# Optimization experiments

Hardware: AMD Instinct MI355X
Metric: run time of the kernel (lower is better)

The kernel has to match this reference:

```python
import jax, jax.numpy as jnp
import numpy as np

B, RES, C = 32, 56, 128
HEADS, WS, NW = 4, 7, 8
HD = C // HEADS            # 32
NQ = NW * NW               # 64 windows
WA = WS * WS               # 49 tokens per window
TOPK = 64


def _topk_closest(q_win, k_win, topk):
    qh, qw = q_win; kh, kw = k_win
    ch_q = np.arange(qh); cw_q = np.arange(qw)
    if qh != kh:
        f = kh // qh
        ch_q = ch_q * f + f // 2
        cw_q = cw_q * f + f // 2
    cq = np.stack(np.meshgrid(ch_q, cw_q, indexing='ij'))              # (2,qh,qw)
    ck = np.stack(np.meshgrid(np.arange(kh), np.arange(kw), indexing='ij'))
    fq = cq.reshape(2, -1); fk = ck.reshape(2, -1)
    rel = fq[:, :, None] - fk[:, None, :]                               # (2,nQ,nK)
    dist = np.sqrt(rel[0].astype(np.float32) ** 2 + rel[1].astype(np.float32) ** 2)
    topk = min(topk, dist.shape[1])
    idx = np.argsort(dist, axis=1, kind='stable')[:, :topk]             # (nQ,topk)
    coord = np.take_along_axis(rel, np.broadcast_to(idx[None], (2,) + idx.shape), axis=2)
    return idx.astype(np.int32), coord.transpose(1, 2, 0).astype(np.float32)


def _buffers():
    # window-relative coords, same as register_buffer('window_coords')
    ch = np.arange(WS) - WS // 2
    wc = np.stack(np.meshgrid(ch, ch, indexing='ij'), axis=-1).reshape(-1, 2).astype(np.float32)  # (49,2)
    # level 0: fine grid (RES x RES); level 1: window grid (NW x NW)
    idx0, c0 = _topk_closest((NW, NW), (RES, RES), TOPK)
    idx1, c1 = _topk_closest((NW, NW), (NW, NW), TOPK)
    c1 = c1 * WS  # k > 0 coords scaled by window size
    coords0 = c0[:, None, :, :] + wc[None, :, None, :]   # (NQ,49,TOPK,2)
    coords1 = c1[:, None, :, :] + wc[None, :, None, :]
    return idx0, idx1, coords0, coords1


def setup_inputs() -> dict:
    key = jax.random.key(0)
    ks = jax.random.split(key, 16)
    idx0, idx1, coords0, coords1 = _buffers()
    s = 0.02
    return {
        'x0': jax.random.normal(ks[0], (B, RES, RES, C), jnp.float32),
        'x1': jax.random.normal(ks[1], (B, NQ, C), jnp.float32),
        'qkv_w': jax.random.normal(ks[2], (3 * C, C), jnp.float32) * s,
        'qkv_b': jnp.zeros((3 * C,), jnp.float32),
        'proj_w': jax.random.normal(ks[3], (C, C), jnp.float32) * s,
        'proj_b': jnp.zeros((C,), jnp.float32),
        'rpb0_w1': jax.random.normal(ks[4], (HD, 2), jnp.float32) * s,
        'rpb0_b1': jnp.zeros((HD,), jnp.float32),
        'rpb0_w2': jax.random.normal(ks[5], (HEADS, HD), jnp.float32) * s,
        'rpb0_b2': jnp.zeros((HEADS,), jnp.float32),
        'rpb1_w1': jax.random.normal(ks[6], (HD, 2), jnp.float32) * s,
        'rpb1_b1': jnp.zeros((HD,), jnp.float32),
        'rpb1_w2': jax.random.normal(ks[7], (HEADS, HD), jnp.float32) * s,
        'rpb1_b2': jnp.zeros((HEADS,), jnp.float32),
        'coords0': jnp.asarray(coords0),
        'coords1': jnp.asarray(coords1),
        'idx0': jnp.asarray(idx0),
        'idx1': jnp.asarray(idx1),
    }


def _rpb_mlp(coords, w1, b1, w2, b2):
    # (NQ,49,T,2) -> (NQ,49,T,heads)
    return jax.nn.relu(coords @ w1.T + b1) @ w2.T + b2


def _gather_kv(kv, idx_flat):
    # kv: (B,L,heads,hd); gathered -> (B,NQ,heads,TOPK,hd)
    g = kv[:, idx_flat]
    return g.reshape(kv.shape[0], NQ, TOPK, HEADS, HD).transpose(0, 1, 3, 2, 4)


def reference(x0, x1, qkv_w, qkv_b, proj_w, proj_b,
              rpb0_w1, rpb0_b1, rpb0_w2, rpb0_b2,
              rpb1_w1, rpb1_b1, rpb1_w2, rpb1_b2,
              coords0, coords1, idx0, idx1):
    b = x0.shape[0]
    scale = HD ** -0.5
    qkv = x0 @ qkv_w.T + qkv_b                       # (B,RES,RES,3C)
    q, k, v = jnp.split(qkv, 3, axis=-1)
    # window-partition q: (B,RES,RES,C) -> (B,NQ,heads,49,hd)
    qw = q.reshape(b, NW, WS, NW, WS, C).transpose(0, 1, 3, 2, 4, 5)
    qw = qw.reshape(b, NQ, WA, HEADS, HD).transpose(0, 1, 3, 2, 4)
    # level 0 KV from fine grid
    k0 = k.reshape(b, RES * RES, HEADS, HD)
    v0 = v.reshape(b, RES * RES, HEADS, HD)
    i0 = idx0.reshape(-1)
    k0s, v0s = _gather_kv(k0, i0), _gather_kv(v0, i0)
    # level 1 KV from pooled tokens (same qkv projection)
    qkv1 = (x1 @ qkv_w.T + qkv_b).reshape(b, NQ, 3, HEADS, HD)
    i1 = idx1.reshape(-1)
    k1s, v1s = _gather_kv(qkv1[:, :, 1], i1), _gather_kv(qkv1[:, :, 2], i1)
    k_all = jnp.concatenate([k0s, k1s], axis=3)      # (B,NQ,heads,2T,hd)
    v_all = jnp.concatenate([v0s, v1s], axis=3)
    attn = jnp.einsum('bqhnd,bqhmd->bqhnm', qw * scale, k_all)  # (B,NQ,heads,49,2T)
    rpb0 = _rpb_mlp(coords0, rpb0_w1, rpb0_b1, rpb0_w2, rpb0_b2)
    rpb1 = _rpb_mlp(coords1, rpb1_w1, rpb1_b1, rpb1_w2, rpb1_b2)
    rpb = jnp.concatenate([rpb0, rpb1], axis=2).transpose(0, 3, 1, 2)  # (NQ,heads,49,2T)
    attn = jax.nn.softmax(attn + rpb[None], axis=-1)
    out = jnp.einsum('bqhnm,bqhmd->bqhnd', attn, v_all)
    out = out.transpose(0, 1, 3, 2, 4).reshape(b * NQ, WA, C)
    return out @ proj_w.T + proj_b
```

## Files before the change

kernel.cpp:

```cpp
#include <hip/hip_runtime.h>
#include <hip/hip_bf16.h>


typedef __bf16 bf16_t;
typedef __bf16 bf16x8 __attribute__((ext_vector_type(8)));
typedef float f32x4 __attribute__((ext_vector_type(4)));

static __device__ __forceinline__ f32x4 mfma_bf16(bf16x8 a, bf16x8 b, f32x4 c) {
  return __builtin_amdgcn_mfma_f32_16x16x32_bf16(a, b, c, 0, 0, 0);
}

static __device__ __forceinline__ bf16x8 cvt8(const float* __restrict__ p) {
  float4 a = *(const float4*)p;
  float4 b = *(const float4*)(p + 4);
  bf16x8 r;
  r[0] = (bf16_t)a.x; r[1] = (bf16_t)a.y; r[2] = (bf16_t)a.z; r[3] = (bf16_t)a.w;
  r[4] = (bf16_t)b.x; r[5] = (bf16_t)b.y; r[6] = (bf16_t)b.z; r[7] = (bf16_t)b.w;
  return r;
}

#define NB 32
#define RES 56
#define CH 128
#define NW 8
#define NQ 64
#define WA 49
#define X0_ROWS (NB * RES * RES)
#define SCALE 0.17677669529663687f
#define SQRT32 5.656854249492381f

__global__ __launch_bounds__(256) void k_qkv(
    const float* __restrict__ x0, const float* __restrict__ x1,
    const float* __restrict__ w, const float* __restrict__ bias,
    bf16_t* __restrict__ qout,
    bf16_t* __restrict__ k0, bf16_t* __restrict__ v0,
    bf16_t* __restrict__ k1, bf16_t* __restrict__ v1) {
  __shared__ __align__(16) bf16_t Asm[64][136];
  __shared__ __align__(16) bf16_t Bsm[128][136];
  const int rb = blockIdx.x;
  const int tid = threadIdx.x;
  const size_t row0 = (size_t)rb * 64;
  const bool is_x0 = (rb < 1568);
  const int b_ = rb / 49;
  const int pix0 = (rb - b_ * 49) * 64;
  const int i1base = (rb - 1568) * 64;

  const float* src = is_x0 ? (x0 + row0 * CH)
                           : (x1 + (row0 - X0_ROWS) * CH);
#pragma unroll
  for (int i = 0; i < 4; ++i) {
    int uid = tid + 256 * i;
    int r = uid >> 4, cs = uid & 15;
    *(bf16x8*)&Asm[r][cs * 8] = cvt8(src + (size_t)r * CH + cs * 8);
  }

  const int wid = tid >> 6, l = tid & 63;
  const int lr = l & 15, lkg = l >> 4, lk = lkg * 8;

  for (int cb = 0; cb < 3; ++cb) {
    const float* wsrc = w + (size_t)cb * 128 * CH;
#pragma unroll
    for (int i = 0; i < 8; ++i) {
      int uid = tid + 256 * i;
      int r = uid >> 4, cs = uid & 15;
      *(bf16x8*)&Bsm[r][cs * 8] = cvt8(wsrc + (size_t)r * CH + cs * 8);
    }
    __syncthreads();

    f32x4 zero = {0.f, 0.f, 0.f, 0.f};
    f32x4 acc[8];
#pragma unroll
    for (int nt = 0; nt < 8; ++nt) acc[nt] = zero;
#pragma unroll
    for (int ks = 0; ks < 4; ++ks) {
      bf16x8 a = *(const bf16x8*)&Asm[wid * 16 + lr][ks * 32 + lk];
#pragma unroll
      for (int nt = 0; nt < 8; ++nt) {
        bf16x8 b = *(const bf16x8*)&Bsm[nt * 16 + lr][ks * 32 + lk];
        acc[nt] = mfma_bf16(a, b, acc[nt]);
      }
    }
    float bias_v[8];
#pragma unroll
    for (int nt = 0; nt < 8; ++nt) bias_v[nt] = bias[cb * 128 + nt * 16 + lr];

#pragma unroll
    for (int r4 = 0; r4 < 4; ++r4) {
      int local = wid * 16 + lkg * 4 + r4;
      if (is_x0) {
        int pix = pix0 + local;
        int rr = pix / 56, cc = pix - rr * 56;
        if (cb == 0) {
          int wn = b_ * 64 + (rr / 7) * 8 + cc / 7;
          int nidx = (rr % 7) * 7 + (cc % 7);
          bf16_t* dst = qout + (size_t)wn * 12544 + nidx * 128;
#pragma unroll
          for (int nt = 0; nt < 8; ++nt)
            dst[nt * 16 + lr] = (bf16_t)(acc[nt][r4] + bias_v[nt]);
        } else {
          bf16_t* dst = (cb == 1 ? k0 : v0) +
                        ((size_t)b_ * 3136 + pix) * CH;
#pragma unroll
          for (int nt = 0; nt < 8; ++nt)
            dst[nt * 16 + lr] = (bf16_t)(acc[nt][r4] + bias_v[nt]);
        }
      } else if (cb != 0) {
        bf16_t* dst = (cb == 1 ? k1 : v1) + (size_t)(i1base + local) * CH;
#pragma unroll
        for (int nt = 0; nt < 8; ++nt)
          dst[nt * 16 + lr] = (bf16_t)(acc[nt][r4] + bias_v[nt]);
      }
    }
    __syncthreads();
  }
}

__global__ __launch_bounds__(256) void k_rpb(
    const float* __restrict__ c0, const float* __restrict__ c1,
    const float* __restrict__ w10, const float* __restrict__ b10,
    const float* __restrict__ w20, const float* __restrict__ b20,
    const float* __restrict__ w11, const float* __restrict__ b11,
    const float* __restrict__ w21, const float* __restrict__ b21,
    float* __restrict__ rpb) {
  __shared__ float w1s[2][32][2], b1s[2][32], w2s[2][4][32], b2s[2][4];
  const int tid = threadIdx.x;
  if (tid < 64) {
    int s = tid >> 5, j = tid & 31;
    const float* w1p = s ? w11 : w10;
    const float* b1p = s ? b11 : b10;
    w1s[s][j][0] = w1p[j * 2];
    w1s[s][j][1] = w1p[j * 2 + 1];
    b1s[s][j] = b1p[j];
  }
  {
    int s = tid >> 7, rem = tid & 127, h = rem >> 5, j = rem & 31;
    w2s[s][h][j] = s ? w21[h * 32 + j] : w20[h * 32 + j];
  }
  if (tid < 8) {
    int s = tid >> 2, h = tid & 3;
    b2s[s][h] = s ? b21[h] : b20[h];
  }
  __syncthreads();

  int L = blockIdx.x * 256 + tid;
  int m = L & 127;
  int n = (L >> 7) % WA;
  int qi = L / (128 * WA);
  int s = m >> 6, mi = m & 63;
  const float* cp = (s ? c1 : c0) + (((size_t)qi * WA + n) * 64 + mi) * 2;
  float cx = cp[0], cy = cp[1];
  float a0 = 0.f, a1 = 0.f, a2 = 0.f, a3 = 0.f;
#pragma unroll
  for (int j = 0; j < 32; ++j) {
    float h = fmaxf(w1s[s][j][0] * cx + w1s[s][j][1] * cy + b1s[s][j], 0.f);
    a0 += w2s[s][0][j] * h;
    a1 += w2s[s][1][j] * h;
    a2 += w2s[s][2][j] * h;
    a3 += w2s[s][3][j] * h;
  }
  size_t base = ((size_t)qi * 4 * WA + n) * 128 + m;
  rpb[base] = (a0 + b2s[s][0]) * SQRT32;
  rpb[base + (size_t)WA * 128] = (a1 + b2s[s][1]) * SQRT32;
  rpb[base + (size_t)2 * WA * 128] = (a2 + b2s[s][2]) * SQRT32;
  rpb[base + (size_t)3 * WA * 128] = (a3 + b2s[s][3]) * SQRT32;
}

__global__ __launch_bounds__(256) void k_attn(
    const bf16_t* qin,
    const bf16_t* __restrict__ k0, const bf16_t* __restrict__ v0,
    const bf16_t* __restrict__ k1, const bf16_t* __restrict__ v1,
    const int* __restrict__ idx0, const int* __restrict__ idx1,
    const float* __restrict__ rpb,
    float* attn_out) {
  __shared__ __align__(16) bf16_t Kt[128][72];
  __shared__ __align__(16) bf16_t Vt[64][136];
  __shared__ __align__(16) bf16_t Sm[64][136];

  const int bid = blockIdx.x;
  const int hp = bid & 1;
  const int qi = (bid >> 1) & 63;
  const int b = bid >> 7;
  const int tid = threadIdx.x;
  const int wn = b * 64 + qi;

#pragma unroll
  for (int i = 0; i < 4; ++i) {
    int uid = tid + 256 * i;
    int key = uid & 127, seg = uid >> 7;
    size_t srcrow;
    const bf16_t *kbase, *vbase;
    if (key < 64) {
      srcrow = (size_t)b * 3136 + idx0[qi * 64 + key];
      kbase = k0; vbase = v0;
    } else {
      srcrow = (size_t)b * 64 + idx1[qi * 64 + key - 64];
      kbase = k1; vbase = v1;
    }
    size_t off = srcrow * CH + hp * 64 + seg * 8;
    *(uint4*)&Kt[key][seg * 8] = *(const uint4*)(kbase + off);
    union { uint4 u; bf16_t h[8]; } cv;
    cv.u = *(const uint4*)(vbase + off);
#pragma unroll
    for (int e = 0; e < 8; ++e) Vt[seg * 8 + e][key] = cv.h[e];
  }

  const int wid = tid >> 6, l = tid & 63;
  const int lr = l & 15, lkg = l >> 4, lk = lkg * 8;
  int qr = wid * 16 + lr;
  if (qr > WA - 1) qr = WA - 1;

  const bf16_t* qb = qin + (size_t)wn * 12544;
  bf16x8 qf[2];
  qf[0] = *(const bf16x8*)&qb[qr * 128 + hp * 64 + lk];
  qf[1] = *(const bf16x8*)&qb[qr * 128 + hp * 64 + 32 + lk];
  __syncthreads();

  const int myrow = wid * 16 + lkg * 4;
  float* obase = attn_out + (size_t)wn * 6272;

#pragma unroll
  for (int lh = 0; lh < 2; ++lh) {
    const int hh = hp * 2 + lh;
    const float* rp = rpb + ((size_t)(qi * 4 + hh) * WA) * 128;
    f32x4 acc[8];
#pragma unroll
    for (int nt = 0; nt < 8; ++nt) {
#pragma unroll
      for (int r4 = 0; r4 < 4; ++r4)
        acc[nt][r4] = rp[(myrow + r4) * 128 + nt * 16 + lr];
    }
#pragma unroll
    for (int nt = 0; nt < 8; ++nt) {
      bf16x8 bfr = *(const bf16x8*)&Kt[nt * 16 + lr][lh * 32 + lk];
      acc[nt] = mfma_bf16(qf[lh], bfr, acc[nt]);
    }
    float mx[4] = {-1e30f, -1e30f, -1e30f, -1e30f};
#pragma unroll
    for (int nt = 0; nt < 8; ++nt)
#pragma unroll
      for (int r4 = 0; r4 < 4; ++r4) mx[r4] = fmaxf(mx[r4], acc[nt][r4]);
#pragma unroll
    for (int m = 1; m < 16; m <<= 1)
#pragma unroll
      for (int r4 = 0; r4 < 4; ++r4)
        mx[r4] = fmaxf(mx[r4], __shfl_xor(mx[r4], m));
    float sum[4] = {0.f, 0.f, 0.f, 0.f};
#pragma unroll
    for (int nt = 0; nt < 8; ++nt)
#pragma unroll
      for (int r4 = 0; r4 < 4; ++r4) {
        float p = __expf(SCALE * (acc[nt][r4] - mx[r4]));
        acc[nt][r4] = p;
        sum[r4] += p;
      }
#pragma unroll
    for (int m = 1; m < 16; m <<= 1)
#pragma unroll
      for (int r4 = 0; r4 < 4; ++r4) sum[r4] += __shfl_xor(sum[r4], m);
#pragma unroll
    for (int nt = 0; nt < 8; ++nt)
#pragma unroll
      for (int r4 = 0; r4 < 4; ++r4)
        Sm[myrow + r4][nt * 16 + lr] = (bf16_t)acc[nt][r4];
    f32x4 zero = {0.f, 0.f, 0.f, 0.f};
    f32x4 oacc[2];
    oacc[0] = zero; oacc[1] = zero;
#pragma unroll
    for (int ks = 0; ks < 4; ++ks) {
      bf16x8 pa = *(const bf16x8*)&Sm[wid * 16 + lr][ks * 32 + lk];
#pragma unroll
      for (int nt2 = 0; nt2 < 2; ++nt2) {
        bf16x8 vb = *(const bf16x8*)&Vt[lh * 32 + nt2 * 16 + lr][ks * 32 + lk];
        oacc[nt2] = mfma_bf16(pa, vb, oacc[nt2]);
      }
    }
#pragma unroll
    for (int nt2 = 0; nt2 < 2; ++nt2)
#pragma unroll
      for (int r4 = 0; r4 < 4; ++r4) {
        int rown = myrow + r4;
        if (rown < WA)
          obase[rown * 128 + hh * 32 + nt2 * 16 + lr] = oacc[nt2][r4] / sum[r4];
      }
  }
}

__global__ __launch_bounds__(256) void k_proj(
    const float* attn,
    const float* __restrict__ pw, const float* __restrict__ pb,
    float* out) {
  __shared__ __align__(16) bf16_t Asm[64][136];
  __shared__ __align__(16) bf16_t Bsm[128][136];
  const int rb = blockIdx.x;
  const int tid = threadIdx.x;
  const size_t row0 = (size_t)rb * 64;
#pragma unroll
  for (int i = 0; i < 4; ++i) {
    int uid = tid + 256 * i;
    int r = uid >> 4, cs = uid & 15;
    *(bf16x8*)&Asm[r][cs * 8] = cvt8(attn + (row0 + r) * CH + cs * 8);
  }
#pragma unroll
  for (int i = 0; i < 8; ++i) {
    int uid = tid + 256 * i;
    int r = uid >> 4, cs = uid & 15;
    *(bf16x8*)&Bsm[r][cs * 8] = cvt8(pw + (size_t)r * CH + cs * 8);
  }
  __syncthreads();

  const int wid = tid >> 6, l = tid & 63;
  const int lr = l & 15, lkg = l >> 4, lk = lkg * 8;
  f32x4 zero = {0.f, 0.f, 0.f, 0.f};
  f32x4 acc[8];
#pragma unroll
  for (int nt = 0; nt < 8; ++nt) acc[nt] = zero;
#pragma unroll
  for (int ks = 0; ks < 4; ++ks) {
    bf16x8 a = *(const bf16x8*)&Asm[wid * 16 + lr][ks * 32 + lk];
#pragma unroll
    for (int nt = 0; nt < 8; ++nt) {
      bf16x8 b = *(const bf16x8*)&Bsm[nt * 16 + lr][ks * 32 + lk];
      acc[nt] = mfma_bf16(a, b, acc[nt]);
    }
  }
#pragma unroll
  for (int nt = 0; nt < 8; ++nt) {
    int n = nt * 16 + lr;
    float bs = pb[n];
#pragma unroll
    for (int r4 = 0; r4 < 4; ++r4) {
      size_t g = row0 + (size_t)(wid * 16 + lkg * 4 + r4);
      out[g * CH + n] = acc[nt][r4] + bs;
    }
  }
}

extern "C" void kernel_launch(void* const* d_in, const int* in_sizes, int n_in,
                              void* d_out, int out_size, void* d_ws, size_t ws_size,
                              hipStream_t stream) {
  const float* x0 = (const float*)d_in[0];
  const float* x1 = (const float*)d_in[1];
  const float* qkv_w = (const float*)d_in[2];
  const float* qkv_b = (const float*)d_in[3];
  const float* proj_w = (const float*)d_in[4];
  const float* proj_b = (const float*)d_in[5];
  const float* rpb0_w1 = (const float*)d_in[6];
  const float* rpb0_b1 = (const float*)d_in[7];
  const float* rpb0_w2 = (const float*)d_in[8];
  const float* rpb0_b2 = (const float*)d_in[9];
  const float* rpb1_w1 = (const float*)d_in[10];
  const float* rpb1_b1 = (const float*)d_in[11];
  const float* rpb1_w2 = (const float*)d_in[12];
  const float* rpb1_b2 = (const float*)d_in[13];
  const float* coords0 = (const float*)d_in[14];
  const float* coords1 = (const float*)d_in[15];
  const int* idx0 = (const int*)d_in[16];
  const int* idx1 = (const int*)d_in[17];

  char* ws = (char*)d_ws;
  bf16_t* k0 = (bf16_t*)(ws + 0);
  bf16_t* v0 = (bf16_t*)(ws + 25690112);
  bf16_t* k1 = (bf16_t*)(ws + 51380224);
  bf16_t* v1 = (bf16_t*)(ws + 51904512);
  float* rpb = (float*)(ws + 52428800);

  k_qkv<<<1600, 256, 0, stream>>>(x0, x1, qkv_w, qkv_b,
                                  (bf16_t*)d_out, k0, v0, k1, v1);
  k_rpb<<<1568, 256, 0, stream>>>(coords0, coords1, rpb0_w1, rpb0_b1, rpb0_w2,
                                  rpb0_b2, rpb1_w1, rpb1_b1, rpb1_w2, rpb1_b2,
                                  rpb);
  k_attn<<<4096, 256, 0, stream>>>((const bf16_t*)d_out, k0, v0, k1, v1,
                                   idx0, idx1, rpb, (float*)d_out);
  k_proj<<<1568, 256, 0, stream>>>((const float*)d_out, proj_w, proj_b,
                                   (float*)d_out);
}
```

Baseline: 228.3 us.

## Fuse output projection into attention and pre-convert weights and RPB to bf16

Adds a prep kernel that converts the qkv and proj weights to bf16 once per call. The rpb table is now stored in bf16, pre-swizzled into the MFMA accumulator layout so it loads as vectors. The qkv GEMM keeps A fragments in registers and stages each output tile through LDS for coalesced 16-byte stores. The attention kernel now handles all four heads of a window per block and applies the output projection in-kernel, which removes the fp32 intermediate round trip and the separate proj launch. The trade-offs are fewer attention blocks (half as many), more LDS per block, and bf16 rounding of the rpb and the attention output before projection.

```diff
diff --git a/kernel.cpp b/kernel.cpp
--- a/kernel.cpp
+++ b/kernel.cpp
@@ -4,6 +4,7 @@
 
 typedef __bf16 bf16_t;
 typedef __bf16 bf16x8 __attribute__((ext_vector_type(8)));
+typedef __bf16 bf16x4 __attribute__((ext_vector_type(4)));
 typedef float f32x4 __attribute__((ext_vector_type(4)));
 
 static __device__ __forceinline__ f32x4 mfma_bf16(bf16x8 a, bf16x8 b, f32x4 c) {
@@ -22,16 +23,76 @@
 #define NB 32
 #define RES 56
 #define CH 128
-#define NW 8
 #define NQ 64
 #define WA 49
 #define X0_ROWS (NB * RES * RES)
 #define SCALE 0.17677669529663687f
 #define SQRT32 5.656854249492381f
 
+__global__ __launch_bounds__(256) void k_prep(
+    const float* __restrict__ qkv_w, const float* __restrict__ proj_w,
+    bf16_t* __restrict__ wq, bf16_t* __restrict__ pwb) {
+  int i = blockIdx.x * 256 + threadIdx.x;
+  if (i < 49152) wq[i] = (bf16_t)qkv_w[i];
+  else if (i - 49152 < 16384) pwb[i - 49152] = (bf16_t)proj_w[i - 49152];
+}
+
+__global__ __launch_bounds__(256) void k_rpb(
+    const float* __restrict__ c0, const float* __restrict__ c1,
+    const float* __restrict__ w10, const float* __restrict__ b10,
+    const float* __restrict__ w20, const float* __restrict__ b20,
+    const float* __restrict__ w11, const float* __restrict__ b11,
+    const float* __restrict__ w21, const float* __restrict__ b21,
+    bf16_t* __restrict__ rpb2) {
+  __shared__ float w1s[2][32][2], b1s[2][32], w2s[2][4][32], b2s[2][4];
+  const int tid = threadIdx.x;
+  if (tid < 64) {
+    int s = tid >> 5, j = tid & 31;
+    const float* w1p = s ? w11 : w10;
+    const float* b1p = s ? b11 : b10;
+    w1s[s][j][0] = w1p[j * 2];
+    w1s[s][j][1] = w1p[j * 2 + 1];
+    b1s[s][j] = b1p[j];
+  }
+  {
+    int s = tid >> 7, rem = tid & 127, h = rem >> 5, j = rem & 31;
+    w2s[s][h][j] = s ? w21[h * 32 + j] : w20[h * 32 + j];
+  }
+  if (tid < 8) {
+    int s = tid >> 2, h = tid & 3;
+    b2s[s][h] = s ? b21[h] : b20[h];
+  }
+  __syncthreads();
+
+  int L = blockIdx.x * 256 + tid;
+  int m = L & 127;
+  int n = (L >> 7) % WA;
+  int qi = L / (128 * WA);
+  int s = m >> 6, mi = m & 63;
+  const float* cp = (s ? c1 : c0) + (((size_t)qi * WA + n) * 64 + mi) * 2;
+  float cx = cp[0], cy = cp[1];
+  float a0 = 0.f, a1 = 0.f, a2 = 0.f, a3 = 0.f;
+#pragma unroll
+  for (int j = 0; j < 32; ++j) {
+    float h = fmaxf(w1s[s][j][0] * cx + w1s[s][j][1] * cy + b1s[s][j], 0.f);
+    a0 += w2s[s][0][j] * h;
+    a1 += w2s[s][1][j] * h;
+    a2 += w2s[s][2][j] * h;
+    a3 += w2s[s][3][j] * h;
+  }
+  int nt = m >> 4, lr = m & 15;
+  int wid2 = n >> 4, lkg2 = (n >> 2) & 3, r4 = n & 3;
+  int t2 = wid2 * 64 + lkg2 * 16 + lr;
+  size_t base2 = (((size_t)(qi * 4) * 8 + nt) * 256 + t2) * 4 + r4;
+  rpb2[base2]         = (bf16_t)((a0 + b2s[s][0]) * SQRT32);
+  rpb2[base2 + 8192]  = (bf16_t)((a1 + b2s[s][1]) * SQRT32);
+  rpb2[base2 + 16384] = (bf16_t)((a2 + b2s[s][2]) * SQRT32);
+  rpb2[base2 + 24576] = (bf16_t)((a3 + b2s[s][3]) * SQRT32);
+}
+
 __global__ __launch_bounds__(256) void k_qkv(
     const float* __restrict__ x0, const float* __restrict__ x1,
-    const float* __restrict__ w, const float* __restrict__ bias,
+    const bf16_t* __restrict__ wq, const float* __restrict__ bias,
     bf16_t* __restrict__ qout,
     bf16_t* __restrict__ k0, bf16_t* __restrict__ v0,
     bf16_t* __restrict__ k1, bf16_t* __restrict__ v1) {
@@ -53,116 +114,80 @@
     int r = uid >> 4, cs = uid & 15;
     *(bf16x8*)&Asm[r][cs * 8] = cvt8(src + (size_t)r * CH + cs * 8);
   }
+#pragma unroll
+  for (int i = 0; i < 8; ++i) {
+    int uid = tid + 256 * i;
+    int r = uid >> 4, cs = uid & 15;
+    *(uint4*)&Bsm[r][cs * 8] = *(const uint4*)(wq + (size_t)r * CH + cs * 8);
+  }
+  __syncthreads();
 
   const int wid = tid >> 6, l = tid & 63;
   const int lr = l & 15, lkg = l >> 4, lk = lkg * 8;
+  const int myrow = wid * 16 + lkg * 4;
+
+  bf16x8 af[4];
+#pragma unroll
+  for (int ks = 0; ks < 4; ++ks)
+    af[ks] = *(const bf16x8*)&Asm[wid * 16 + lr][ks * 32 + lk];
 
   for (int cb = 0; cb < 3; ++cb) {
-    const float* wsrc = w + (size_t)cb * 128 * CH;
-#pragma unroll
-    for (int i = 0; i < 8; ++i) {
-      int uid = tid + 256 * i;
-      int r = uid >> 4, cs = uid & 15;
-      *(bf16x8*)&Bsm[r][cs * 8] = cvt8(wsrc + (size_t)r * CH + cs * 8);
-    }
-    __syncthreads();
-
     f32x4 zero = {0.f, 0.f, 0.f, 0.f};
     f32x4 acc[8];
 #pragma unroll
     for (int nt = 0; nt < 8; ++nt) acc[nt] = zero;
 #pragma unroll
-    for (int ks = 0; ks < 4; ++ks) {
-      bf16x8 a = *(const bf16x8*)&Asm[wid * 16 + lr][ks * 32 + lk];
+    for (int ks = 0; ks < 4; ++ks)
 #pragma unroll
       for (int nt = 0; nt < 8; ++nt) {
         bf16x8 b = *(const bf16x8*)&Bsm[nt * 16 + lr][ks * 32 + lk];
-        acc[nt] = mfma_bf16(a, b, acc[nt]);
-      }
-    }
-    float bias_v[8];
-#pragma unroll
-    for (int nt = 0; nt < 8; ++nt) bias_v[nt] = bias[cb * 128 + nt * 16 + lr];
-
-#pragma unroll
-    for (int r4 = 0; r4 < 4; ++r4) {
-      int local = wid * 16 + lkg * 4 + r4;
-      if (is_x0) {
-        int pix = pix0 + local;
-        int rr = pix / 56, cc = pix - rr * 56;
-        if (cb == 0) {
+        acc[nt] = mfma_bf16(af[ks], b, acc[nt]);
+      }
+    __syncthreads();
+
+    const bool emit = is_x0 || cb != 0;
+    if (emit) {
+#pragma unroll
+      for (int nt = 0; nt < 8; ++nt) {
+        float bs = bias[cb * 128 + nt * 16 + lr];
+#pragma unroll
+        for (int r4 = 0; r4 < 4; ++r4)
+          Asm[myrow + r4][nt * 16 + lr] = (bf16_t)(acc[nt][r4] + bs);
+      }
+    }
+    __syncthreads();
+
+    if (cb < 2) {
+#pragma unroll
+      for (int i = 0; i < 8; ++i) {
+        int uid = tid + 256 * i;
+        int r = uid >> 4, cs = uid & 15;
+        *(uint4*)&Bsm[r][cs * 8] =
+            *(const uint4*)(wq + (size_t)(cb + 1) * 16384 + r * CH + cs * 8);
+      }
+    }
+    if (emit) {
+#pragma unroll
+      for (int i = 0; i < 4; ++i) {
+        int uid = tid + 256 * i;
+        int r = uid >> 4, cs = uid & 15;
+        bf16_t* dptr;
+        if (!is_x0) {
+          dptr = (cb == 1 ? k1 : v1) + (size_t)(i1base + r) * CH;
+        } else if (cb == 0) {
+          int pix = pix0 + r;
+          int rr = pix / 56, cc = pix - rr * 56;
           int wn = b_ * 64 + (rr / 7) * 8 + cc / 7;
-          int nidx = (rr % 7) * 7 + (cc % 7);
-          bf16_t* dst = qout + (size_t)wn * 12544 + nidx * 128;
-#pragma unroll
-          for (int nt = 0; nt < 8; ++nt)
-            dst[nt * 16 + lr] = (bf16_t)(acc[nt][r4] + bias_v[nt]);
+          int nid = (rr % 7) * 7 + (cc % 7);
+          dptr = qout + (size_t)wn * 12544 + nid * 128;
         } else {
-          bf16_t* dst = (cb == 1 ? k0 : v0) +
-                        ((size_t)b_ * 3136 + pix) * CH;
-#pragma unroll
-          for (int nt = 0; nt < 8; ++nt)
-            dst[nt * 16 + lr] = (bf16_t)(acc[nt][r4] + bias_v[nt]);
+          dptr = (cb == 1 ? k0 : v0) + (row0 + r) * CH;
         }
-      } else if (cb != 0) {
-        bf16_t* dst = (cb == 1 ? k1 : v1) + (size_t)(i1base + local) * CH;
-#pragma unroll
-        for (int nt = 0; nt < 8; ++nt)
-          dst[nt * 16 + lr] = (bf16_t)(acc[nt][r4] + bias_v[nt]);
-      }
-    }
-    __syncthreads();
-  }
-}
-
-__global__ __launch_bounds__(256) void k_rpb(
-    const float* __restrict__ c0, const float* __restrict__ c1,
-    const float* __restrict__ w10, const float* __restrict__ b10,
-    const float* __restrict__ w20, const float* __restrict__ b20,
-    const float* __restrict__ w11, const float* __restrict__ b11,
-    const float* __restrict__ w21, const float* __restrict__ b21,
-    float* __restrict__ rpb) {
-  __shared__ float w1s[2][32][2], b1s[2][32], w2s[2][4][32], b2s[2][4];
-  const int tid = threadIdx.x;
-  if (tid < 64) {
-    int s = tid >> 5, j = tid & 31;
-    const float* w1p = s ? w11 : w10;
-    const float* b1p = s ? b11 : b10;
-    w1s[s][j][0] = w1p[j * 2];
-    w1s[s][j][1] = w1p[j * 2 + 1];
-    b1s[s][j] = b1p[j];
-  }
-  {
-    int s = tid >> 7, rem = tid & 127, h = rem >> 5, j = rem & 31;
-    w2s[s][h][j] = s ? w21[h * 32 + j] : w20[h * 32 + j];
-  }
-  if (tid < 8) {
-    int s = tid >> 2, h = tid & 3;
-    b2s[s][h] = s ? b21[h] : b20[h];
-  }
-  __syncthreads();
-
-  int L = blockIdx.x * 256 + tid;
-  int m = L & 127;
-  int n = (L >> 7) % WA;
-  int qi = L / (128 * WA);
-  int s = m >> 6, mi = m & 63;
-  const float* cp = (s ? c1 : c0) + (((size_t)qi * WA + n) * 64 + mi) * 2;
-  float cx = cp[0], cy = cp[1];
-  float a0 = 0.f, a1 = 0.f, a2 = 0.f, a3 = 0.f;
-#pragma unroll
-  for (int j = 0; j < 32; ++j) {
-    float h = fmaxf(w1s[s][j][0] * cx + w1s[s][j][1] * cy + b1s[s][j], 0.f);
-    a0 += w2s[s][0][j] * h;
-    a1 += w2s[s][1][j] * h;
-    a2 += w2s[s][2][j] * h;
-    a3 += w2s[s][3][j] * h;
-  }
-  size_t base = ((size_t)qi * 4 * WA + n) * 128 + m;
-  rpb[base] = (a0 + b2s[s][0]) * SQRT32;
-  rpb[base + (size_t)WA * 128] = (a1 + b2s[s][1]) * SQRT32;
-  rpb[base + (size_t)2 * WA * 128] = (a2 + b2s[s][2]) * SQRT32;
-  rpb[base + (size_t)3 * WA * 128] = (a3 + b2s[s][3]) * SQRT32;
+        *(uint4*)(dptr + cs * 8) = *(const uint4*)&Asm[r][cs * 8];
+      }
+    }
+    __syncthreads();
+  }
 }
 
 __global__ __launch_bounds__(256) void k_attn(
@@ -170,167 +195,162 @@
     const bf16_t* __restrict__ k0, const bf16_t* __restrict__ v0,
     const bf16_t* __restrict__ k1, const bf16_t* __restrict__ v1,
     const int* __restrict__ idx0, const int* __restrict__ idx1,
-    const float* __restrict__ rpb,
+    const bf16_t* __restrict__ rpb2, const bf16_t* __restrict__ pw,
+    const float* __restrict__ pb,
     float* attn_out) {
-  __shared__ __align__(16) bf16_t Kt[128][72];
-  __shared__ __align__(16) bf16_t Vt[64][136];
-  __shared__ __align__(16) bf16_t Sm[64][136];
+  __shared__ __align__(16) char smem[53248];
+  bf16_t* Kt = (bf16_t*)smem;
+  bf16_t* Vt = (bf16_t*)(smem + 18432);
+  bf16_t* Sm = (bf16_t*)(smem + 35840);
+  bf16_t* Om = (bf16_t*)smem;
+  bf16_t* Pw = (bf16_t*)(smem + 18432);
 
   const int bid = blockIdx.x;
-  const int hp = bid & 1;
-  const int qi = (bid >> 1) & 63;
-  const int b = bid >> 7;
+  const int qi = bid & 63;
+  const int b = bid >> 6;
   const int tid = threadIdx.x;
-  const int wn = b * 64 + qi;
-
-#pragma unroll
-  for (int i = 0; i < 4; ++i) {
-    int uid = tid + 256 * i;
-    int key = uid & 127, seg = uid >> 7;
-    size_t srcrow;
-    const bf16_t *kbase, *vbase;
-    if (key < 64) {
-      srcrow = (size_t)b * 3136 + idx0[qi * 64 + key];
-      kbase = k0; vbase = v0;
-    } else {
-      srcrow = (size_t)b * 64 + idx1[qi * 64 + key - 64];
-      kbase = k1; vbase = v1;
-    }
-    size_t off = srcrow * CH + hp * 64 + seg * 8;
-    *(uint4*)&Kt[key][seg * 8] = *(const uint4*)(kbase + off);
-    union { uint4 u; bf16_t h[8]; } cv;
-    cv.u = *(const uint4*)(vbase + off);
-#pragma unroll
-    for (int e = 0; e < 8; ++e) Vt[seg * 8 + e][key] = cv.h[e];
-  }
+  const int wn = bid;
 
   const int wid = tid >> 6, l = tid & 63;
   const int lr = l & 15, lkg = l >> 4, lk = lkg * 8;
+  const int myrow = wid * 16 + lkg * 4;
   int qr = wid * 16 + lr;
   if (qr > WA - 1) qr = WA - 1;
-
   const bf16_t* qb = qin + (size_t)wn * 12544;
-  bf16x8 qf[2];
-  qf[0] = *(const bf16x8*)&qb[qr * 128 + hp * 64 + lk];
-  qf[1] = *(const bf16x8*)&qb[qr * 128 + hp * 64 + 32 + lk];
-  __syncthreads();
-
-  const int myrow = wid * 16 + lkg * 4;
-  float* obase = attn_out + (size_t)wn * 6272;
-
-#pragma unroll
-  for (int lh = 0; lh < 2; ++lh) {
-    const int hh = hp * 2 + lh;
-    const float* rp = rpb + ((size_t)(qi * 4 + hh) * WA) * 128;
-    f32x4 acc[8];
-#pragma unroll
-    for (int nt = 0; nt < 8; ++nt) {
+
+  f32x4 oreg[4][2];
+  float rsum[4][4];
+
+  for (int p = 0; p < 2; ++p) {
+#pragma unroll
+    for (int i = 0; i < 4; ++i) {
+      int uid = tid + 256 * i;
+      int key = uid & 127, seg = uid >> 7;
+      size_t srcrow;
+      const bf16_t *kbase, *vbase;
+      if (key < 64) {
+        srcrow = (size_t)b * 3136 + idx0[qi * 64 + key];
+        kbase = k0; vbase = v0;
+      } else {
+        srcrow = (size_t)b * 64 + idx1[qi * 64 + key - 64];
+        kbase = k1; vbase = v1;
+      }
+      size_t off = srcrow * CH + p * 64 + seg * 8;
+      *(uint4*)&Kt[key * 72 + seg * 8] = *(const uint4*)(kbase + off);
+      union { uint4 u; bf16_t h[8]; } cv;
+      cv.u = *(const uint4*)(vbase + off);
+#pragma unroll
+      for (int e = 0; e < 8; ++e) Vt[(seg * 8 + e) * 136 + key] = cv.h[e];
+    }
+    bf16x8 qf[2];
+    qf[0] = *(const bf16x8*)&qb[qr * 128 + p * 64 + lk];
+    qf[1] = *(const bf16x8*)&qb[qr * 128 + p * 64 + 32 + lk];
+    __syncthreads();
+
+#pragma unroll
+    for (int lh = 0; lh < 2; ++lh) {
+      const int hh = p * 2 + lh;
+      const bf16_t* rp = rpb2 + (((size_t)(qi * 4 + hh)) * 8) * 1024 + tid * 4;
+      f32x4 acc[8];
+#pragma unroll
+      for (int nt = 0; nt < 8; ++nt) {
+        bf16x4 v = *(const bf16x4*)(rp + nt * 1024);
+        acc[nt][0] = (float)v[0]; acc[nt][1] = (float)v[1];
+        acc[nt][2] = (float)v[2]; acc[nt][3] = (float)v[3];
+      }
+#pragma unroll
+      for (int nt = 0; nt < 8; ++nt) {
+        bf16x8 bfr = *(const bf16x8*)&Kt[(nt * 16 + lr) * 72 + lh * 32 + lk];
+        acc[nt] = mfma_bf16(qf[lh], bfr, acc[nt]);
+      }
+      float mx[4] = {-1e30f, -1e30f, -1e30f, -1e30f};
+#pragma unroll
+      for (int nt = 0; nt < 8; ++nt)
+#pragma unroll
+        for (int r4 = 0; r4 < 4; ++r4) mx[r4] = fmaxf(mx[r4], acc[nt][r4]);
+#pragma unroll
+      for (int m = 1; m < 16; m <<= 1)
+#pragma unroll
+        for (int r4 = 0; r4 < 4; ++r4)
+          mx[r4] = fmaxf(mx[r4], __shfl_xor(mx[r4], m));
+      float sum[4] = {0.f, 0.f, 0.f, 0.f};
+#pragma unroll
+      for (int nt = 0; nt < 8; ++nt)
+#pragma unroll
+        for (int r4 = 0; r4 < 4; ++r4) {
+          float pv = __expf(SCALE * (acc[nt][r4] - mx[r4]));
+          acc[nt][r4] = pv;
+          sum[r4] += pv;
+        }
+#pragma unroll
+      for (int m = 1; m < 16; m <<= 1)
+#pragma unroll
+        for (int r4 = 0; r4 < 4; ++r4) sum[r4] += __shfl_xor(sum[r4], m);
 #pragma unroll
       for (int r4 = 0; r4 < 4; ++r4)
-        acc[nt][r4] = rp[(myrow + r4) * 128 + nt * 16 + lr];
-    }
-#pragma unroll
-    for (int nt = 0; nt < 8; ++nt) {
-      bf16x8 bfr = *(const bf16x8*)&Kt[nt * 16 + lr][lh * 32 + lk];
-      acc[nt] = mfma_bf16(qf[lh], bfr, acc[nt]);
-    }
-    float mx[4] = {-1e30f, -1e30f, -1e30f, -1e30f};
-#pragma unroll
-    for (int nt = 0; nt < 8; ++nt)
-#pragma unroll
-      for (int r4 = 0; r4 < 4; ++r4) mx[r4] = fmaxf(mx[r4], acc[nt][r4]);
-#pragma unroll
-    for (int m = 1; m < 16; m <<= 1)
+        rsum[hh][r4] = __builtin_amdgcn_rcpf(sum[r4]);
+#pragma unroll
+      for (int nt = 0; nt < 8; ++nt)
+#pragma unroll
+        for (int r4 = 0; r4 < 4; ++r4)
+          Sm[(myrow + r4) * 136 + nt * 16 + lr] = (bf16_t)acc[nt][r4];
+      f32x4 zero = {0.f, 0.f, 0.f, 0.f};
+      f32x4 oacc[2];
+      oacc[0] = zero; oacc[1] = zero;
+#pragma unroll
+      for (int ks = 0; ks < 4; ++ks) {
+        bf16x8 pa = *(const bf16x8*)&Sm[(wid * 16 + lr) * 136 + ks * 32 + lk];
+#pragma unroll
+        for (int nt2 = 0; nt2 < 2; ++nt2) {
+          bf16x8 vb = *(const bf16x8*)
+              &Vt[(lh * 32 + nt2 * 16 + lr) * 136 + ks * 32 + lk];
+          oacc[nt2] = mfma_bf16(pa, vb, oacc[nt2]);
+        }
+      }
+      oreg[hh][0] = oacc[0];
+      oreg[hh][1] = oacc[1];
+    }
+    __syncthreads();
+  }
+
+#pragma unroll
+  for (int hh = 0; hh < 4; ++hh)
+#pragma unroll
+    for (int nt2 = 0; nt2 < 2; ++nt2)
 #pragma unroll
       for (int r4 = 0; r4 < 4; ++r4)
-        mx[r4] = fmaxf(mx[r4], __shfl_xor(mx[r4], m));
-    float sum[4] = {0.f, 0.f, 0.f, 0.f};
-#pragma unroll
-    for (int nt = 0; nt < 8; ++nt)
-#pragma unroll
-      for (int r4 = 0; r4 < 4; ++r4) {
-        float p = __expf(SCALE * (acc[nt][r4] - mx[r4]));
-        acc[nt][r4] = p;
-        sum[r4] += p;
-      }
-#pragma unroll
-    for (int m = 1; m < 16; m <<= 1)
-#pragma unroll
-      for (int r4 = 0; r4 < 4; ++r4) sum[r4] += __shfl_xor(sum[r4], m);
-#pragma unroll
-    for (int nt = 0; nt < 8; ++nt)
-#pragma unroll
-      for (int r4 = 0; r4 < 4; ++r4)
-        Sm[myrow + r4][nt * 16 + lr] = (bf16_t)acc[nt][r4];
-    f32x4 zero = {0.f, 0.f, 0.f, 0.f};
-    f32x4 oacc[2];
-    oacc[0] = zero; oacc[1] = zero;
-#pragma unroll
-    for (int ks = 0; ks < 4; ++ks) {
-      bf16x8 pa = *(const bf16x8*)&Sm[wid * 16 + lr][ks * 32 + lk];
-#pragma unroll
-      for (int nt2 = 0; nt2 < 2; ++nt2) {
-        bf16x8 vb = *(const bf16x8*)&Vt[lh * 32 + nt2 * 16 + lr][ks * 32 + lk];
-        oacc[nt2] = mfma_bf16(pa, vb, oacc[nt2]);
-      }
-    }
-#pragma unroll
-    for (int nt2 = 0; nt2 < 2; ++nt2)
-#pragma unroll
-      for (int r4 = 0; r4 < 4; ++r4) {
-        int rown = myrow + r4;
-        if (rown < WA)
-          obase[rown * 128 + hh * 32 + nt2 * 16 + lr] = oacc[nt2][r4] / sum[r4];
-      }
-  }
-}
-
-__global__ __launch_bounds__(256) void k_proj(
-    const float* attn,
-    const float* __restrict__ pw, const float* __restrict__ pb,
-    float* out) {
-  __shared__ __align__(16) bf16_t Asm[64][136];
-  __shared__ __align__(16) bf16_t Bsm[128][136];
-  const int rb = blockIdx.x;
-  const int tid = threadIdx.x;
-  const size_t row0 = (size_t)rb * 64;
-#pragma unroll
-  for (int i = 0; i < 4; ++i) {
-    int uid = tid + 256 * i;
-    int r = uid >> 4, cs = uid & 15;
-    *(bf16x8*)&Asm[r][cs * 8] = cvt8(attn + (row0 + r) * CH + cs * 8);
-  }
+        Om[(myrow + r4) * 136 + hh * 32 + nt2 * 16 + lr] =
+            (bf16_t)(oreg[hh][nt2][r4] * rsum[hh][r4]);
 #pragma unroll
   for (int i = 0; i < 8; ++i) {
     int uid = tid + 256 * i;
     int r = uid >> 4, cs = uid & 15;
-    *(bf16x8*)&Bsm[r][cs * 8] = cvt8(pw + (size_t)r * CH + cs * 8);
+    *(uint4*)&Pw[r * 136 + cs * 8] = *(const uint4*)(pw + r * CH + cs * 8);
   }
   __syncthreads();
 
-  const int wid = tid >> 6, l = tid & 63;
-  const int lr = l & 15, lkg = l >> 4, lk = lkg * 8;
   f32x4 zero = {0.f, 0.f, 0.f, 0.f};
   f32x4 acc[8];
 #pragma unroll
   for (int nt = 0; nt < 8; ++nt) acc[nt] = zero;
 #pragma unroll
   for (int ks = 0; ks < 4; ++ks) {
-    bf16x8 a = *(const bf16x8*)&Asm[wid * 16 + lr][ks * 32 + lk];
+    bf16x8 a = *(const bf16x8*)&Om[(wid * 16 + lr) * 136 + ks * 32 + lk];
 #pragma unroll
     for (int nt = 0; nt < 8; ++nt) {
-      bf16x8 b = *(const bf16x8*)&Bsm[nt * 16 + lr][ks * 32 + lk];
-      acc[nt] = mfma_bf16(a, b, acc[nt]);
-    }
-  }
+      bf16x8 bfr = *(const bf16x8*)&Pw[(nt * 16 + lr) * 136 + ks * 32 + lk];
+      acc[nt] = mfma_bf16(a, bfr, acc[nt]);
+    }
+  }
+  float* obase = attn_out + (size_t)wn * 6272;
 #pragma unroll
   for (int nt = 0; nt < 8; ++nt) {
-    int n = nt * 16 + lr;
-    float bs = pb[n];
+    float bs = pb[nt * 16 + lr];
 #pragma unroll
     for (int r4 = 0; r4 < 4; ++r4) {
-      size_t g = row0 + (size_t)(wid * 16 + lkg * 4 + r4);
-      out[g * CH + n] = acc[nt][r4] + bs;
+      int rown = myrow + r4;
+      if (rown < WA)
+        obase[rown * 128 + nt * 16 + lr] = acc[nt][r4] + bs;
     }
   }
 }
@@ -362,15 +382,17 @@
   bf16_t* v0 = (bf16_t*)(ws + 25690112);
   bf16_t* k1 = (bf16_t*)(ws + 51380224);
   bf16_t* v1 = (bf16_t*)(ws + 51904512);
-  float* rpb = (float*)(ws + 52428800);
-
-  k_qkv<<<1600, 256, 0, stream>>>(x0, x1, qkv_w, qkv_b,
-                                  (bf16_t*)d_out, k0, v0, k1, v1);
+  bf16_t* rpb2 = (bf16_t*)(ws + 52428800);
+  bf16_t* wq = (bf16_t*)(ws + 56623104);
+  bf16_t* pwb = (bf16_t*)(ws + 56721408);
+
+  k_prep<<<256, 256, 0, stream>>>(qkv_w, proj_w, wq, pwb);
   k_rpb<<<1568, 256, 0, stream>>>(coords0, coords1, rpb0_w1, rpb0_b1, rpb0_w2,
                                   rpb0_b2, rpb1_w1, rpb1_b1, rpb1_w2, rpb1_b2,
-                                  rpb);
-  k_attn<<<4096, 256, 0, stream>>>((const bf16_t*)d_out, k0, v0, k1, v1,
-                                   idx0, idx1, rpb, (float*)d_out);
-  k_proj<<<1568, 256, 0, stream>>>((const float*)d_out, proj_w, proj_b,
+                                  rpb2);
+  k_qkv<<<1600, 256, 0, stream>>>(x0, x1, wq, qkv_b,
+                                  (bf16_t*)d_out, k0, v0, k1, v1);
+  k_attn<<<2048, 256, 0, stream>>>((const bf16_t*)d_out, k0, v0, k1, v1,
+                                   idx0, idx1, rpb2, pwb, proj_b,
                                    (float*)d_out);
 }
```

Measured after the change: 234.8 us. +2.8%, slower.
